# Optimization experiments

Measured on AMD Instinct MI355X. Metric: run time of the kernel, lower is better.

The kernel has to match this reference:

```python
import jax, jax.numpy as jnp
import numpy as np

NUM_FIELDS = 26

def setup_inputs() -> dict:
    key = jax.random.key(0)
    ks = jax.random.split(key, 8)
    B, F, D, V, d, af = 4096, NUM_FIELDS, 13, 100000, 64, 64
    return {
        "sparse_feat": jax.random.randint(ks[0], (B, F), 0, V, dtype=jnp.int32),
        "dense_feat": jax.random.uniform(ks[1], (B, D), dtype=jnp.float32),
        "embed_table": jax.random.normal(ks[2], (V, d), dtype=jnp.float32) * 0.05,
        "lin_table": jax.random.normal(ks[3], (V,), dtype=jnp.float32) * 0.05,
        "w_dense": jax.random.normal(ks[4], (D,), dtype=jnp.float32) * 0.1,
        "bias": jnp.zeros((1,), dtype=jnp.float32),
        "W1": jax.random.normal(ks[5], (d, af), dtype=jnp.float32) * (1.0 / np.sqrt(d)),
        "b1": jnp.zeros((af,), dtype=jnp.float32),
        "w2": jax.random.normal(ks[6], (af,), dtype=jnp.float32) * (1.0 / np.sqrt(af)),
        "p": jax.random.normal(ks[7], (d,), dtype=jnp.float32) * (1.0 / np.sqrt(d)),
    }

def reference(sparse_feat, dense_feat, embed_table, lin_table, w_dense, bias, W1, b1, w2, p):
    # Embedding lookup: [B, F, d]
    emb = embed_table[sparse_feat]
    # Linear part: per-field scalar weights + dense linear + bias -> [B]
    linear_out = lin_table[sparse_feat].sum(axis=1) + dense_feat @ w_dense + bias[0]
    # Pairwise interactions i<j (static indices): [B, P, d]
    i_idx, j_idx = np.triu_indices(NUM_FIELDS, k=1)
    att_x = emb[:, i_idx, :] * emb[:, j_idx, :]
    # Attention MLP: Linear(d, af) + ReLU + Linear(af, 1, no bias) -> [B, P]
    h = jax.nn.relu(jnp.einsum('bpd,da->bpa', att_x, W1) + b1)
    att_w = jnp.einsum('bpa,a->bp', h, w2)
    att_score = jax.nn.softmax(att_w, axis=1)
    # Softmax-weighted sum over pairs -> [B, d], then final projection p -> [B]
    att_out = jnp.einsum('bpd,bp->bd', att_x, att_score)
    fm_att_out = att_out @ p
    return linear_out + fm_att_out
```

## Files before the change

### kernel.cpp

```cpp
#include <hip/hip_runtime.h>
#include <math.h>


#define NF 26
#define NP 325
#define NMT 21
#define ED 64
#define AF 64
#define NDENSE 13
#define WPB 4
#define BLOCK (WPB * 64)
#define ESTRIDE 72
#define WSTRIDE 72

typedef __attribute__((ext_vector_type(8))) _Float16 half8;
typedef __attribute__((ext_vector_type(4))) float f32x4;

__global__ __launch_bounds__(BLOCK, 4)
void afm_kernel(const int*   __restrict__ sparse,
                const float* __restrict__ dense,
                const float* __restrict__ etab,
                const float* __restrict__ ltab,
                const float* __restrict__ wdense,
                const float* __restrict__ bias,
                const float* __restrict__ W1,
                const float* __restrict__ b1,
                const float* __restrict__ w2,
                const float* __restrict__ proj,
                float*       __restrict__ out,
                int B)
{
    const int t    = threadIdx.x;
    const int wave = t >> 6;
    const int lane = t & 63;
    const int qd   = lane >> 4;
    const int ln   = lane & 15;

    __shared__ alignas(16) _Float16       w1t_s[AF][WSTRIDE];
    __shared__              unsigned short tab_s[NMT * 16];
    __shared__ alignas(16) _Float16       emb_all[WPB][NF][ESTRIDE];

    for (int idx = t; idx < ED * AF; idx += BLOCK) {
        int d = idx >> 6, a = idx & 63;
        w1t_s[a][d] = (_Float16)W1[idx];
    }
    for (int p = t; p < NMT * 16; p += BLOCK) {
        unsigned short v = 0;
        if (p < NP) {
            int rem = p, i = 0;
            while (rem >= NF - 1 - i) { rem -= NF - 1 - i; ++i; }
            v = (unsigned short)(i | ((i + 1 + rem) << 8));
        }
        tab_s[p] = v;
    }

    const int r = blockIdx.x * WPB + wave;
    const bool active = (r < B);

    _Float16 (* __restrict__ emb)[ESTRIDE] = emb_all[wave];
    float lin = 0.f;
    float4 b1v4[4], w2v4[4];

    if (active) {
        const int* __restrict__ srow = sparse + r * NF;
        for (int task = lane; task < NF * 8; task += 64) {
            int f = task >> 3, c = task & 7;
            const float* src = etab + (size_t)srow[f] * ED + c * 8;
            float4 v0 = *(const float4*)(src);
            float4 v1 = *(const float4*)(src + 4);
            half8 h = { (_Float16)v0.x, (_Float16)v0.y, (_Float16)v0.z, (_Float16)v0.w,
                        (_Float16)v1.x, (_Float16)v1.y, (_Float16)v1.z, (_Float16)v1.w };
            *(half8*)(&emb[f][c * 8]) = h;
        }

        #pragma unroll
        for (int nt = 0; nt < 4; ++nt) {
            b1v4[nt] = *(const float4*)(b1 + nt * 16 + qd * 4);
            w2v4[nt] = *(const float4*)(w2 + nt * 16 + qd * 4);
        }

        if (lane < NF) {
            lin = ltab[srow[lane]];
        } else if (lane >= 32 && lane < 32 + NDENSE) {
            int k = lane - 32;
            lin = dense[r * NDENSE + k] * wdense[k];
        }
        #pragma unroll
        for (int off = 32; off >= 1; off >>= 1) lin += __shfl_xor(lin, off, 64);
        lin += bias[0];
    }

    __syncthreads();
    if (!active) return;

    half8 bfr[4][2];
    #pragma unroll
    for (int nt = 0; nt < 4; ++nt)
        #pragma unroll
        for (int kh = 0; kh < 2; ++kh)
            bfr[nt][kh] = *(const half8*)(&w1t_s[nt * 16 + ln][kh * 32 + qd * 8]);

    float m = -INFINITY, l = 0.f;
    half8 acc0 = { (_Float16)0.f, (_Float16)0.f, (_Float16)0.f, (_Float16)0.f,
                   (_Float16)0.f, (_Float16)0.f, (_Float16)0.f, (_Float16)0.f };
    half8 acc1 = acc0;

    unsigned pp = tab_s[ln];
    int fi = pp & 0xff, fj = pp >> 8;
    half8 ei0 = *(const half8*)(&emb[fi][qd * 8]);
    half8 ei1 = *(const half8*)(&emb[fi][32 + qd * 8]);
    half8 ej0 = *(const half8*)(&emb[fj][qd * 8]);
    half8 ej1 = *(const half8*)(&emb[fj][32 + qd * 8]);

    for (int mt = 0; mt < NMT; ++mt) {
        half8 x0 = ei0 * ej0;
        half8 x1 = ei1 * ej1;

        if (mt + 1 < NMT) {
            unsigned np = tab_s[(mt + 1) * 16 + ln];
            int nfi = np & 0xff, nfj = np >> 8;
            ei0 = *(const half8*)(&emb[nfi][qd * 8]);
            ei1 = *(const half8*)(&emb[nfi][32 + qd * 8]);
            ej0 = *(const half8*)(&emb[nfj][qd * 8]);
            ej1 = *(const half8*)(&emb[nfj][32 + qd * 8]);
        }

        float lgp[4];
        #pragma unroll
        for (int nt = 0; nt < 4; ++nt) {
            f32x4 acc = { b1v4[nt].x, b1v4[nt].y, b1v4[nt].z, b1v4[nt].w };
            acc = __builtin_amdgcn_mfma_f32_16x16x32_f16(bfr[nt][0], x0, acc, 0, 0, 0);
            acc = __builtin_amdgcn_mfma_f32_16x16x32_f16(bfr[nt][1], x1, acc, 0, 0, 0);
            float u = fmaf(fmaxf(acc[1], 0.f), w2v4[nt].y, fmaxf(acc[0], 0.f) * w2v4[nt].x);
            float v = fmaf(fmaxf(acc[3], 0.f), w2v4[nt].w, fmaxf(acc[2], 0.f) * w2v4[nt].z);
            lgp[nt] = u + v;
        }
        float lg = (lgp[0] + lgp[1]) + (lgp[2] + lgp[3]);
        lg += __shfl_xor(lg, 16, 64);
        lg += __shfl_xor(lg, 32, 64);

        const int p0 = mt * 16 + ln;
        if (p0 >= NP) lg = -INFINITY;

        float mn    = fmaxf(m, lg);
        float alpha = __expf(m - mn);
        float e     = __expf(lg - mn);
        l = l * alpha + e;
        m = mn;
        _Float16 ah = (_Float16)alpha, eh = (_Float16)e;
        half8 a8 = { ah, ah, ah, ah, ah, ah, ah, ah };
        half8 e8 = { eh, eh, eh, eh, eh, eh, eh, eh };
        acc0 = acc0 * a8 + x0 * e8;
        acc1 = acc1 * a8 + x1 * e8;
    }

    float mg = m;
    #pragma unroll
    for (int off = 1; off <= 8; off <<= 1) mg = fmaxf(mg, __shfl_xor(mg, off, 64));
    const float fac = __expf(m - mg);
    float lsum = l * fac;
    #pragma unroll
    for (int off = 1; off <= 8; off <<= 1) lsum += __shfl_xor(lsum, off, 64);

    float4 pa = *(const float4*)(proj + qd * 8);
    float4 pb = *(const float4*)(proj + qd * 8 + 4);
    float4 pc = *(const float4*)(proj + 32 + qd * 8);
    float4 pd = *(const float4*)(proj + 32 + qd * 8 + 4);
    float rr = (float)acc0[0] * pa.x + (float)acc0[1] * pa.y
             + (float)acc0[2] * pa.z + (float)acc0[3] * pa.w
             + (float)acc0[4] * pb.x + (float)acc0[5] * pb.y
             + (float)acc0[6] * pb.z + (float)acc0[7] * pb.w
             + (float)acc1[0] * pc.x + (float)acc1[1] * pc.y
             + (float)acc1[2] * pc.z + (float)acc1[3] * pc.w
             + (float)acc1[4] * pd.x + (float)acc1[5] * pd.y
             + (float)acc1[6] * pd.z + (float)acc1[7] * pd.w;
    rr *= fac;
    #pragma unroll
    for (int off = 1; off <= 32; off <<= 1) rr += __shfl_xor(rr, off, 64);

    if (lane == 0) out[r] = lin + rr / lsum;
}

extern "C" void kernel_launch(void* const* d_in, const int* in_sizes, int n_in,
                              void* d_out, int out_size, void* d_ws, size_t ws_size,
                              hipStream_t stream) {
    const int*   sparse = (const int*)  d_in[0];
    const float* dense  = (const float*)d_in[1];
    const float* etab   = (const float*)d_in[2];
    const float* ltab   = (const float*)d_in[3];
    const float* wdense = (const float*)d_in[4];
    const float* bias   = (const float*)d_in[5];
    const float* W1     = (const float*)d_in[6];
    const float* b1     = (const float*)d_in[7];
    const float* w2     = (const float*)d_in[8];
    const float* proj   = (const float*)d_in[9];
    float* outp = (float*)d_out;

    const int B = in_sizes[0] / NF;

    afm_kernel<<<dim3((B + WPB - 1) / WPB), dim3(BLOCK), 0, stream>>>(
        sparse, dense, etab, ltab, wdense, bias, W1, b1, w2, proj, outp, B);
    (void)n_in; (void)out_size; (void)d_ws; (void)ws_size;
}
```

Baseline: 113.0 us.

## Process two pair tiles per iteration and gather embeddings block-wide

The pair loop now handles two 16-pair tiles per iteration, issuing eight independent MFMAs and doing one online-softmax rescale per pair of tiles. This is meant to raise instruction-level parallelism and halve the softmax/exp overhead, at the cost of dropping the explicit next-tile LDS prefetch and using more registers. The embedding gather is moved to a block-strided loop over all four rows, spreading the loads across all threads before the W1 transpose. The tile count grows from 21 to 22, with the extra tile masked to -inf.

```diff
diff --git a/kernel.cpp b/kernel.cpp
--- a/kernel.cpp
+++ b/kernel.cpp
@@ -4,7 +4,8 @@
 
 #define NF 26
 #define NP 325
-#define NMT 21
+#define NIT 11
+#define NTILE (NIT * 2)
 #define ED 64
 #define AF 64
 #define NDENSE 13
@@ -15,6 +16,12 @@
 
 typedef __attribute__((ext_vector_type(8))) _Float16 half8;
 typedef __attribute__((ext_vector_type(4))) float f32x4;
+
+__device__ __forceinline__ half8 bcast8(float v) {
+    _Float16 h = (_Float16)v;
+    half8 r = { h, h, h, h, h, h, h, h };
+    return r;
+}
 
 __global__ __launch_bounds__(BLOCK, 4)
 void afm_kernel(const int*   __restrict__ sparse,
@@ -37,14 +44,29 @@
     const int ln   = lane & 15;
 
     __shared__ alignas(16) _Float16       w1t_s[AF][WSTRIDE];
-    __shared__              unsigned short tab_s[NMT * 16];
+    __shared__              unsigned short tab_s[NTILE * 16];
     __shared__ alignas(16) _Float16       emb_all[WPB][NF][ESTRIDE];
+
+    for (int task = t; task < WPB * NF * 8; task += BLOCK) {
+        int w   = task / (NF * 8);
+        int rem = task - w * (NF * 8);
+        int f = rem >> 3, c = rem & 7;
+        int rw = blockIdx.x * WPB + w;
+        if (rw < B) {
+            const float* src = etab + (size_t)sparse[rw * NF + f] * ED + c * 8;
+            float4 v0 = *(const float4*)(src);
+            float4 v1 = *(const float4*)(src + 4);
+            half8 h = { (_Float16)v0.x, (_Float16)v0.y, (_Float16)v0.z, (_Float16)v0.w,
+                        (_Float16)v1.x, (_Float16)v1.y, (_Float16)v1.z, (_Float16)v1.w };
+            *(half8*)(&emb_all[w][f][c * 8]) = h;
+        }
+    }
 
     for (int idx = t; idx < ED * AF; idx += BLOCK) {
         int d = idx >> 6, a = idx & 63;
         w1t_s[a][d] = (_Float16)W1[idx];
     }
-    for (int p = t; p < NMT * 16; p += BLOCK) {
+    for (int p = t; p < NTILE * 16; p += BLOCK) {
         unsigned short v = 0;
         if (p < NP) {
             int rem = p, i = 0;
@@ -62,25 +84,13 @@
     float4 b1v4[4], w2v4[4];
 
     if (active) {
-        const int* __restrict__ srow = sparse + r * NF;
-        for (int task = lane; task < NF * 8; task += 64) {
-            int f = task >> 3, c = task & 7;
-            const float* src = etab + (size_t)srow[f] * ED + c * 8;
-            float4 v0 = *(const float4*)(src);
-            float4 v1 = *(const float4*)(src + 4);
-            half8 h = { (_Float16)v0.x, (_Float16)v0.y, (_Float16)v0.z, (_Float16)v0.w,
-                        (_Float16)v1.x, (_Float16)v1.y, (_Float16)v1.z, (_Float16)v1.w };
-            *(half8*)(&emb[f][c * 8]) = h;
-        }
-
         #pragma unroll
         for (int nt = 0; nt < 4; ++nt) {
             b1v4[nt] = *(const float4*)(b1 + nt * 16 + qd * 4);
             w2v4[nt] = *(const float4*)(w2 + nt * 16 + qd * 4);
         }
-
         if (lane < NF) {
-            lin = ltab[srow[lane]];
+            lin = ltab[sparse[r * NF + lane]];
         } else if (lane >= 32 && lane < 32 + NDENSE) {
             int k = lane - 32;
             lin = dense[r * NDENSE + k] * wdense[k];
@@ -101,57 +111,58 @@
             bfr[nt][kh] = *(const half8*)(&w1t_s[nt * 16 + ln][kh * 32 + qd * 8]);
 
     float m = -INFINITY, l = 0.f;
-    half8 acc0 = { (_Float16)0.f, (_Float16)0.f, (_Float16)0.f, (_Float16)0.f,
-                   (_Float16)0.f, (_Float16)0.f, (_Float16)0.f, (_Float16)0.f };
-    half8 acc1 = acc0;
-
-    unsigned pp = tab_s[ln];
-    int fi = pp & 0xff, fj = pp >> 8;
-    half8 ei0 = *(const half8*)(&emb[fi][qd * 8]);
-    half8 ei1 = *(const half8*)(&emb[fi][32 + qd * 8]);
-    half8 ej0 = *(const half8*)(&emb[fj][qd * 8]);
-    half8 ej1 = *(const half8*)(&emb[fj][32 + qd * 8]);
-
-    for (int mt = 0; mt < NMT; ++mt) {
-        half8 x0 = ei0 * ej0;
-        half8 x1 = ei1 * ej1;
-
-        if (mt + 1 < NMT) {
-            unsigned np = tab_s[(mt + 1) * 16 + ln];
-            int nfi = np & 0xff, nfj = np >> 8;
-            ei0 = *(const half8*)(&emb[nfi][qd * 8]);
-            ei1 = *(const half8*)(&emb[nfi][32 + qd * 8]);
-            ej0 = *(const half8*)(&emb[nfj][qd * 8]);
-            ej1 = *(const half8*)(&emb[nfj][32 + qd * 8]);
-        }
-
-        float lgp[4];
+    half8 acc0 = bcast8(0.f), acc1 = bcast8(0.f);
+
+    for (int it = 0; it < NIT; ++it) {
+        const int pa = it * 32 + ln;
+        const int pb = pa + 16;
+        unsigned ppa = tab_s[pa];
+        unsigned ppb = tab_s[pb];
+
+        int fia = ppa & 0xff, fja = ppa >> 8;
+        half8 xa0 = *(const half8*)(&emb[fia][qd * 8])      * *(const half8*)(&emb[fja][qd * 8]);
+        half8 xa1 = *(const half8*)(&emb[fia][32 + qd * 8]) * *(const half8*)(&emb[fja][32 + qd * 8]);
+        int fib = ppb & 0xff, fjb = ppb >> 8;
+        half8 xb0 = *(const half8*)(&emb[fib][qd * 8])      * *(const half8*)(&emb[fjb][qd * 8]);
+        half8 xb1 = *(const half8*)(&emb[fib][32 + qd * 8]) * *(const half8*)(&emb[fjb][32 + qd * 8]);
+
+        float lgpa[4], lgpb[4];
         #pragma unroll
         for (int nt = 0; nt < 4; ++nt) {
-            f32x4 acc = { b1v4[nt].x, b1v4[nt].y, b1v4[nt].z, b1v4[nt].w };
-            acc = __builtin_amdgcn_mfma_f32_16x16x32_f16(bfr[nt][0], x0, acc, 0, 0, 0);
-            acc = __builtin_amdgcn_mfma_f32_16x16x32_f16(bfr[nt][1], x1, acc, 0, 0, 0);
-            float u = fmaf(fmaxf(acc[1], 0.f), w2v4[nt].y, fmaxf(acc[0], 0.f) * w2v4[nt].x);
-            float v = fmaf(fmaxf(acc[3], 0.f), w2v4[nt].w, fmaxf(acc[2], 0.f) * w2v4[nt].z);
-            lgp[nt] = u + v;
-        }
-        float lg = (lgp[0] + lgp[1]) + (lgp[2] + lgp[3]);
-        lg += __shfl_xor(lg, 16, 64);
-        lg += __shfl_xor(lg, 32, 64);
-
-        const int p0 = mt * 16 + ln;
-        if (p0 >= NP) lg = -INFINITY;
-
-        float mn    = fmaxf(m, lg);
+            f32x4 ca = { b1v4[nt].x, b1v4[nt].y, b1v4[nt].z, b1v4[nt].w };
+            ca = __builtin_amdgcn_mfma_f32_16x16x32_f16(bfr[nt][0], xa0, ca, 0, 0, 0);
+            ca = __builtin_amdgcn_mfma_f32_16x16x32_f16(bfr[nt][1], xa1, ca, 0, 0, 0);
+            f32x4 cb = { b1v4[nt].x, b1v4[nt].y, b1v4[nt].z, b1v4[nt].w };
+            cb = __builtin_amdgcn_mfma_f32_16x16x32_f16(bfr[nt][0], xb0, cb, 0, 0, 0);
+            cb = __builtin_amdgcn_mfma_f32_16x16x32_f16(bfr[nt][1], xb1, cb, 0, 0, 0);
+            float ua = fmaf(fmaxf(ca[1], 0.f), w2v4[nt].y, fmaxf(ca[0], 0.f) * w2v4[nt].x);
+            float va = fmaf(fmaxf(ca[3], 0.f), w2v4[nt].w, fmaxf(ca[2], 0.f) * w2v4[nt].z);
+            lgpa[nt] = ua + va;
+            float ub = fmaf(fmaxf(cb[1], 0.f), w2v4[nt].y, fmaxf(cb[0], 0.f) * w2v4[nt].x);
+            float vb = fmaf(fmaxf(cb[3], 0.f), w2v4[nt].w, fmaxf(cb[2], 0.f) * w2v4[nt].z);
+            lgpb[nt] = ub + vb;
+        }
+        float lga = (lgpa[0] + lgpa[1]) + (lgpa[2] + lgpa[3]);
+        float lgb = (lgpb[0] + lgpb[1]) + (lgpb[2] + lgpb[3]);
+        lga += __shfl_xor(lga, 16, 64);
+        lga += __shfl_xor(lga, 32, 64);
+        lgb += __shfl_xor(lgb, 16, 64);
+        lgb += __shfl_xor(lgb, 32, 64);
+
+        if (pa >= NP) lga = -INFINITY;
+        if (pb >= NP) lgb = -INFINITY;
+
+        float mn    = fmaxf(fmaxf(m, lga), lgb);
         float alpha = __expf(m - mn);
-        float e     = __expf(lg - mn);
-        l = l * alpha + e;
+        float ea    = __expf(lga - mn);
+        float eb    = __expf(lgb - mn);
+        l = l * alpha + ea + eb;
         m = mn;
-        _Float16 ah = (_Float16)alpha, eh = (_Float16)e;
-        half8 a8 = { ah, ah, ah, ah, ah, ah, ah, ah };
-        half8 e8 = { eh, eh, eh, eh, eh, eh, eh, eh };
-        acc0 = acc0 * a8 + x0 * e8;
-        acc1 = acc1 * a8 + x1 * e8;
+        half8 a8  = bcast8(alpha);
+        half8 ea8 = bcast8(ea);
+        half8 eb8 = bcast8(eb);
+        acc0 = (acc0 * a8 + xa0 * ea8) + xb0 * eb8;
+        acc1 = (acc1 * a8 + xa1 * ea8) + xb1 * eb8;
     }
 
     float mg = m;
@@ -162,18 +173,18 @@
     #pragma unroll
     for (int off = 1; off <= 8; off <<= 1) lsum += __shfl_xor(lsum, off, 64);
 
-    float4 pa = *(const float4*)(proj + qd * 8);
-    float4 pb = *(const float4*)(proj + qd * 8 + 4);
-    float4 pc = *(const float4*)(proj + 32 + qd * 8);
-    float4 pd = *(const float4*)(proj + 32 + qd * 8 + 4);
-    float rr = (float)acc0[0] * pa.x + (float)acc0[1] * pa.y
-             + (float)acc0[2] * pa.z + (float)acc0[3] * pa.w
-             + (float)acc0[4] * pb.x + (float)acc0[5] * pb.y
-             + (float)acc0[6] * pb.z + (float)acc0[7] * pb.w
-             + (float)acc1[0] * pc.x + (float)acc1[1] * pc.y
-             + (float)acc1[2] * pc.z + (float)acc1[3] * pc.w
-             + (float)acc1[4] * pd.x + (float)acc1[5] * pd.y
-             + (float)acc1[6] * pd.z + (float)acc1[7] * pd.w;
+    float4 pa4 = *(const float4*)(proj + qd * 8);
+    float4 pb4 = *(const float4*)(proj + qd * 8 + 4);
+    float4 pc4 = *(const float4*)(proj + 32 + qd * 8);
+    float4 pd4 = *(const float4*)(proj + 32 + qd * 8 + 4);
+    float rr = (float)acc0[0] * pa4.x + (float)acc0[1] * pa4.y
+             + (float)acc0[2] * pa4.z + (float)acc0[3] * pa4.w
+             + (float)acc0[4] * pb4.x + (float)acc0[5] * pb4.y
+             + (float)acc0[6] * pb4.z + (float)acc0[7] * pb4.w
+             + (float)acc1[0] * pc4.x + (float)acc1[1] * pc4.y
+             + (float)acc1[2] * pc4.z + (float)acc1[3] * pc4.w
+             + (float)acc1[4] * pd4.x + (float)acc1[5] * pd4.y
+             + (float)acc1[6] * pd4.z + (float)acc1[7] * pd4.w;
     rr *= fac;
     #pragma unroll
     for (int off = 1; off <= 32; off <<= 1) rr += __shfl_xor(rr, off, 64);
```

After: 121.4 us. 1.07x slower.

## Split each row's pair tiles across two waves and merge softmax partials

Applied to the files above, without the earlier changes.

Each block now handles two rows instead of four, and each row's 21 pair tiles (padded to 22) are split between two waves of 11 tiles each. The waves combine their online-softmax partials (max, sum, weighted projection) through shared memory after a second barrier. Embedding staging is done cooperatively by the whole block. The aim is to halve the serial per-wave loop latency and double the grid size, at the cost of loading W1 into LDS twice as often overall plus an extra sync and a cross-wave merge.

```diff
diff --git a/kernel.cpp b/kernel.cpp
--- a/kernel.cpp
+++ b/kernel.cpp
@@ -4,10 +4,12 @@
 
 #define NF 26
 #define NP 325
-#define NMT 21
+#define NHT 11
+#define NTILE 22
 #define ED 64
 #define AF 64
 #define NDENSE 13
+#define RPB 2
 #define WPB 4
 #define BLOCK (WPB * 64)
 #define ESTRIDE 72
@@ -15,6 +17,12 @@
 
 typedef __attribute__((ext_vector_type(8))) _Float16 half8;
 typedef __attribute__((ext_vector_type(4))) float f32x4;
+
+__device__ __forceinline__ half8 bcast8(float v) {
+    _Float16 hh = (_Float16)v;
+    half8 r = { hh, hh, hh, hh, hh, hh, hh, hh };
+    return r;
+}
 
 __global__ __launch_bounds__(BLOCK, 4)
 void afm_kernel(const int*   __restrict__ sparse,
@@ -35,16 +43,33 @@
     const int lane = t & 63;
     const int qd   = lane >> 4;
     const int ln   = lane & 15;
+    const int lr   = wave >> 1;
+    const int h    = wave & 1;
 
     __shared__ alignas(16) _Float16       w1t_s[AF][WSTRIDE];
-    __shared__              unsigned short tab_s[NMT * 16];
-    __shared__ alignas(16) _Float16       emb_all[WPB][NF][ESTRIDE];
-
+    __shared__              unsigned short tab_s[NTILE * 16];
+    __shared__ alignas(16) _Float16       emb_all[RPB][NF][ESTRIDE];
+    __shared__              float          red_s[WPB][4];
+
+    for (int task = t; task < RPB * NF * 8; task += BLOCK) {
+        int w   = task / (NF * 8);
+        int rem = task - w * (NF * 8);
+        int f = rem >> 3, c = rem & 7;
+        int rw = blockIdx.x * RPB + w;
+        if (rw < B) {
+            const float* src = etab + (size_t)sparse[rw * NF + f] * ED + c * 8;
+            float4 v0 = *(const float4*)(src);
+            float4 v1 = *(const float4*)(src + 4);
+            half8 hv = { (_Float16)v0.x, (_Float16)v0.y, (_Float16)v0.z, (_Float16)v0.w,
+                         (_Float16)v1.x, (_Float16)v1.y, (_Float16)v1.z, (_Float16)v1.w };
+            *(half8*)(&emb_all[w][f][c * 8]) = hv;
+        }
+    }
     for (int idx = t; idx < ED * AF; idx += BLOCK) {
         int d = idx >> 6, a = idx & 63;
         w1t_s[a][d] = (_Float16)W1[idx];
     }
-    for (int p = t; p < NMT * 16; p += BLOCK) {
+    for (int p = t; p < NTILE * 16; p += BLOCK) {
         unsigned short v = 0;
         if (p < NP) {
             int rem = p, i = 0;
@@ -54,131 +79,133 @@
         tab_s[p] = v;
     }
 
-    const int r = blockIdx.x * WPB + wave;
+    const int r = blockIdx.x * RPB + lr;
     const bool active = (r < B);
 
-    _Float16 (* __restrict__ emb)[ESTRIDE] = emb_all[wave];
+    _Float16 (* __restrict__ emb)[ESTRIDE] = emb_all[lr];
     float lin = 0.f;
-    float4 b1v4[4], w2v4[4];
+
+    __syncthreads();
 
     if (active) {
-        const int* __restrict__ srow = sparse + r * NF;
-        for (int task = lane; task < NF * 8; task += 64) {
-            int f = task >> 3, c = task & 7;
-            const float* src = etab + (size_t)srow[f] * ED + c * 8;
-            float4 v0 = *(const float4*)(src);
-            float4 v1 = *(const float4*)(src + 4);
-            half8 h = { (_Float16)v0.x, (_Float16)v0.y, (_Float16)v0.z, (_Float16)v0.w,
-                        (_Float16)v1.x, (_Float16)v1.y, (_Float16)v1.z, (_Float16)v1.w };
-            *(half8*)(&emb[f][c * 8]) = h;
-        }
-
+        if (h == 0) {
+            if (lane < NF) {
+                lin = ltab[sparse[r * NF + lane]];
+            } else if (lane >= 32 && lane < 32 + NDENSE) {
+                int k = lane - 32;
+                lin = dense[r * NDENSE + k] * wdense[k];
+            }
+            #pragma unroll
+            for (int off = 32; off >= 1; off >>= 1) lin += __shfl_xor(lin, off, 64);
+            lin += bias[0];
+        }
+
+        float4 b1v4[4], w2v4[4];
         #pragma unroll
         for (int nt = 0; nt < 4; ++nt) {
             b1v4[nt] = *(const float4*)(b1 + nt * 16 + qd * 4);
             w2v4[nt] = *(const float4*)(w2 + nt * 16 + qd * 4);
         }
 
-        if (lane < NF) {
-            lin = ltab[srow[lane]];
-        } else if (lane >= 32 && lane < 32 + NDENSE) {
-            int k = lane - 32;
-            lin = dense[r * NDENSE + k] * wdense[k];
-        }
-        #pragma unroll
-        for (int off = 32; off >= 1; off >>= 1) lin += __shfl_xor(lin, off, 64);
-        lin += bias[0];
+        half8 bfr[4][2];
+        #pragma unroll
+        for (int nt = 0; nt < 4; ++nt)
+            #pragma unroll
+            for (int kh = 0; kh < 2; ++kh)
+                bfr[nt][kh] = *(const half8*)(&w1t_s[nt * 16 + ln][kh * 32 + qd * 8]);
+
+        const int tbase = h * NHT;
+        float m = -INFINITY, l = 0.f;
+        half8 acc0 = bcast8(0.f), acc1 = bcast8(0.f);
+
+        unsigned pp = tab_s[tbase * 16 + ln];
+        int fi = pp & 0xff, fj = pp >> 8;
+        half8 ei0 = *(const half8*)(&emb[fi][qd * 8]);
+        half8 ei1 = *(const half8*)(&emb[fi][32 + qd * 8]);
+        half8 ej0 = *(const half8*)(&emb[fj][qd * 8]);
+        half8 ej1 = *(const half8*)(&emb[fj][32 + qd * 8]);
+
+        for (int k = 0; k < NHT; ++k) {
+            half8 x0 = ei0 * ej0;
+            half8 x1 = ei1 * ej1;
+
+            if (k + 1 < NHT) {
+                unsigned np = tab_s[(tbase + k + 1) * 16 + ln];
+                int nfi = np & 0xff, nfj = np >> 8;
+                ei0 = *(const half8*)(&emb[nfi][qd * 8]);
+                ei1 = *(const half8*)(&emb[nfi][32 + qd * 8]);
+                ej0 = *(const half8*)(&emb[nfj][qd * 8]);
+                ej1 = *(const half8*)(&emb[nfj][32 + qd * 8]);
+            }
+
+            float lgp[4];
+            #pragma unroll
+            for (int nt = 0; nt < 4; ++nt) {
+                f32x4 acc = { b1v4[nt].x, b1v4[nt].y, b1v4[nt].z, b1v4[nt].w };
+                acc = __builtin_amdgcn_mfma_f32_16x16x32_f16(bfr[nt][0], x0, acc, 0, 0, 0);
+                acc = __builtin_amdgcn_mfma_f32_16x16x32_f16(bfr[nt][1], x1, acc, 0, 0, 0);
+                float u = fmaf(fmaxf(acc[1], 0.f), w2v4[nt].y, fmaxf(acc[0], 0.f) * w2v4[nt].x);
+                float v = fmaf(fmaxf(acc[3], 0.f), w2v4[nt].w, fmaxf(acc[2], 0.f) * w2v4[nt].z);
+                lgp[nt] = u + v;
+            }
+            float lg = (lgp[0] + lgp[1]) + (lgp[2] + lgp[3]);
+            lg += __shfl_xor(lg, 16, 64);
+            lg += __shfl_xor(lg, 32, 64);
+
+            const int p0 = (tbase + k) * 16 + ln;
+            if (p0 >= NP) lg = -INFINITY;
+
+            float mn    = fmaxf(m, lg);
+            float alpha = __expf(m - mn);
+            float e     = __expf(lg - mn);
+            l = l * alpha + e;
+            m = mn;
+            half8 a8 = bcast8(alpha);
+            half8 e8 = bcast8(e);
+            acc0 = acc0 * a8 + x0 * e8;
+            acc1 = acc1 * a8 + x1 * e8;
+        }
+
+        float mg = m;
+        #pragma unroll
+        for (int off = 1; off <= 8; off <<= 1) mg = fmaxf(mg, __shfl_xor(mg, off, 64));
+        const float fac = __expf(m - mg);
+        float lsum = l * fac;
+        #pragma unroll
+        for (int off = 1; off <= 8; off <<= 1) lsum += __shfl_xor(lsum, off, 64);
+
+        float4 pa4 = *(const float4*)(proj + qd * 8);
+        float4 pb4 = *(const float4*)(proj + qd * 8 + 4);
+        float4 pc4 = *(const float4*)(proj + 32 + qd * 8);
+        float4 pd4 = *(const float4*)(proj + 32 + qd * 8 + 4);
+        float rr = (float)acc0[0] * pa4.x + (float)acc0[1] * pa4.y
+                 + (float)acc0[2] * pa4.z + (float)acc0[3] * pa4.w
+                 + (float)acc0[4] * pb4.x + (float)acc0[5] * pb4.y
+                 + (float)acc0[6] * pb4.z + (float)acc0[7] * pb4.w
+                 + (float)acc1[0] * pc4.x + (float)acc1[1] * pc4.y
+                 + (float)acc1[2] * pc4.z + (float)acc1[3] * pc4.w
+                 + (float)acc1[4] * pd4.x + (float)acc1[5] * pd4.y
+                 + (float)acc1[6] * pd4.z + (float)acc1[7] * pd4.w;
+        rr *= fac;
+        #pragma unroll
+        for (int off = 1; off <= 32; off <<= 1) rr += __shfl_xor(rr, off, 64);
+
+        if (lane == 0) {
+            red_s[wave][0] = mg;
+            red_s[wave][1] = lsum;
+            red_s[wave][2] = rr;
+        }
     }
 
     __syncthreads();
-    if (!active) return;
-
-    half8 bfr[4][2];
-    #pragma unroll
-    for (int nt = 0; nt < 4; ++nt)
-        #pragma unroll
-        for (int kh = 0; kh < 2; ++kh)
-            bfr[nt][kh] = *(const half8*)(&w1t_s[nt * 16 + ln][kh * 32 + qd * 8]);
-
-    float m = -INFINITY, l = 0.f;
-    half8 acc0 = { (_Float16)0.f, (_Float16)0.f, (_Float16)0.f, (_Float16)0.f,
-                   (_Float16)0.f, (_Float16)0.f, (_Float16)0.f, (_Float16)0.f };
-    half8 acc1 = acc0;
-
-    unsigned pp = tab_s[ln];
-    int fi = pp & 0xff, fj = pp >> 8;
-    half8 ei0 = *(const half8*)(&emb[fi][qd * 8]);
-    half8 ei1 = *(const half8*)(&emb[fi][32 + qd * 8]);
-    half8 ej0 = *(const half8*)(&emb[fj][qd * 8]);
-    half8 ej1 = *(const half8*)(&emb[fj][32 + qd * 8]);
-
-    for (int mt = 0; mt < NMT; ++mt) {
-        half8 x0 = ei0 * ej0;
-        half8 x1 = ei1 * ej1;
-
-        if (mt + 1 < NMT) {
-            unsigned np = tab_s[(mt + 1) * 16 + ln];
-            int nfi = np & 0xff, nfj = np >> 8;
-            ei0 = *(const half8*)(&emb[nfi][qd * 8]);
-            ei1 = *(const half8*)(&emb[nfi][32 + qd * 8]);
-            ej0 = *(const half8*)(&emb[nfj][qd * 8]);
-            ej1 = *(const half8*)(&emb[nfj][32 + qd * 8]);
-        }
-
-        float lgp[4];
-        #pragma unroll
-        for (int nt = 0; nt < 4; ++nt) {
-            f32x4 acc = { b1v4[nt].x, b1v4[nt].y, b1v4[nt].z, b1v4[nt].w };
-            acc = __builtin_amdgcn_mfma_f32_16x16x32_f16(bfr[nt][0], x0, acc, 0, 0, 0);
-            acc = __builtin_amdgcn_mfma_f32_16x16x32_f16(bfr[nt][1], x1, acc, 0, 0, 0);
-            float u = fmaf(fmaxf(acc[1], 0.f), w2v4[nt].y, fmaxf(acc[0], 0.f) * w2v4[nt].x);
-            float v = fmaf(fmaxf(acc[3], 0.f), w2v4[nt].w, fmaxf(acc[2], 0.f) * w2v4[nt].z);
-            lgp[nt] = u + v;
-        }
-        float lg = (lgp[0] + lgp[1]) + (lgp[2] + lgp[3]);
-        lg += __shfl_xor(lg, 16, 64);
-        lg += __shfl_xor(lg, 32, 64);
-
-        const int p0 = mt * 16 + ln;
-        if (p0 >= NP) lg = -INFINITY;
-
-        float mn    = fmaxf(m, lg);
-        float alpha = __expf(m - mn);
-        float e     = __expf(lg - mn);
-        l = l * alpha + e;
-        m = mn;
-        _Float16 ah = (_Float16)alpha, eh = (_Float16)e;
-        half8 a8 = { ah, ah, ah, ah, ah, ah, ah, ah };
-        half8 e8 = { eh, eh, eh, eh, eh, eh, eh, eh };
-        acc0 = acc0 * a8 + x0 * e8;
-        acc1 = acc1 * a8 + x1 * e8;
-    }
-
-    float mg = m;
-    #pragma unroll
-    for (int off = 1; off <= 8; off <<= 1) mg = fmaxf(mg, __shfl_xor(mg, off, 64));
-    const float fac = __expf(m - mg);
-    float lsum = l * fac;
-    #pragma unroll
-    for (int off = 1; off <= 8; off <<= 1) lsum += __shfl_xor(lsum, off, 64);
-
-    float4 pa = *(const float4*)(proj + qd * 8);
-    float4 pb = *(const float4*)(proj + qd * 8 + 4);
-    float4 pc = *(const float4*)(proj + 32 + qd * 8);
-    float4 pd = *(const float4*)(proj + 32 + qd * 8 + 4);
-    float rr = (float)acc0[0] * pa.x + (float)acc0[1] * pa.y
-             + (float)acc0[2] * pa.z + (float)acc0[3] * pa.w
-             + (float)acc0[4] * pb.x + (float)acc0[5] * pb.y
-             + (float)acc0[6] * pb.z + (float)acc0[7] * pb.w
-             + (float)acc1[0] * pc.x + (float)acc1[1] * pc.y
-             + (float)acc1[2] * pc.z + (float)acc1[3] * pc.w
-             + (float)acc1[4] * pd.x + (float)acc1[5] * pd.y
-             + (float)acc1[6] * pd.z + (float)acc1[7] * pd.w;
-    rr *= fac;
-    #pragma unroll
-    for (int off = 1; off <= 32; off <<= 1) rr += __shfl_xor(rr, off, 64);
-
-    if (lane == 0) out[r] = lin + rr / lsum;
+
+    if (active && h == 0 && lane == 0) {
+        float m0 = red_s[wave][0],     l0 = red_s[wave][1],     r0 = red_s[wave][2];
+        float m1 = red_s[wave + 1][0], l1 = red_s[wave + 1][1], r1 = red_s[wave + 1][2];
+        float mg = fmaxf(m0, m1);
+        float f0 = __expf(m0 - mg), f1 = __expf(m1 - mg);
+        out[r] = lin + (r0 * f0 + r1 * f1) / (l0 * f0 + l1 * f1);
+    }
 }
 
 extern "C" void kernel_launch(void* const* d_in, const int* in_sizes, int n_in,
@@ -198,7 +225,7 @@
 
     const int B = in_sizes[0] / NF;
 
-    afm_kernel<<<dim3((B + WPB - 1) / WPB), dim3(BLOCK), 0, stream>>>(
+    afm_kernel<<<dim3((B + RPB - 1) / RPB), dim3(BLOCK), 0, stream>>>(
         sparse, dense, etab, ltab, wdense, bias, W1, b1, w2, proj, outp, B);
     (void)n_in; (void)out_size; (void)d_ws; (void)ws_size;
 }
```

Measured after the change: 359.8 us. 3.19x slower.
